# Kernel tuning notes

Hardware: AMD Instinct MI355X
Metric: run time of the kernel (lower is better)

Reference implementation:

```python
import jax, jax.numpy as jnp
import numpy as np

DK, DV, DMODEL, HEADNUM = 64, 64, 1024, 16
SEQ = 4096


def setup_inputs() -> dict:
    key = jax.random.key(0)
    ks = jax.random.split(key, 7)
    s = 0.02
    return {
        "q": jax.random.normal(ks[0], (SEQ, DMODEL), dtype=jnp.float32),
        "k": jax.random.normal(ks[1], (SEQ, DMODEL), dtype=jnp.float32),
        "v": jax.random.normal(ks[2], (SEQ, DMODEL), dtype=jnp.float32),
        # per-head projection weights, stored batched: [H, dmodel, dk]
        "Wq": jax.random.normal(ks[3], (HEADNUM, DMODEL, DK), dtype=jnp.float32) * s,
        "Wk": jax.random.normal(ks[4], (HEADNUM, DMODEL, DK), dtype=jnp.float32) * s,
        "Wv": jax.random.normal(ks[5], (HEADNUM, DMODEL, DV), dtype=jnp.float32) * s,
        # output linear (torch Linear weight [out, in]; y = x @ W.T)
        "Wo": jax.random.normal(ks[6], (DK * HEADNUM, DK * HEADNUM), dtype=jnp.float32) * s,
    }


def reference(q, k, v, Wq, Wk, Wv, Wo):
    # batched per-head projections: [H, S, dk/dv]
    qh = jnp.einsum("sd,hdk->hsk", q, Wq)
    kh = jnp.einsum("sd,hdk->hsk", k, Wk)
    vh = jnp.einsum("sd,hdv->hsv", v, Wv)
    scale = 1.0 / jnp.sqrt(jnp.asarray(DK, dtype=qh.dtype))
    scores = jnp.einsum("hqk,hsk->hqs", qh, kh) * scale  # [H, S, S]
    attn = jax.nn.softmax(scores, axis=-1)
    heads = jnp.einsum("hqs,hsv->hqv", attn, vh)  # [H, S, dv]
    # concat heads along feature dim: [S, H*dv]
    head_cat = jnp.transpose(heads, (1, 0, 2)).reshape(SEQ, HEADNUM * DV)
    return head_cat @ Wo.T
```

## Files before the change

### kernel.cpp

```cpp
#include <hip/hip_runtime.h>

#define SEQ 4096
#define DMODEL 1024
#define HEADNUM 16
#define DHEAD 64

typedef __attribute__((ext_vector_type(8))) short short8;
typedef __attribute__((ext_vector_type(4))) float f32x4;
typedef __attribute__((ext_vector_type(16))) float f32x16;
typedef __attribute__((ext_vector_type(4))) int i32x4;

__device__ __forceinline__ short f2bf(float f) {
    unsigned u = __float_as_uint(f);
    u = (u + 0x7fffu + ((u >> 16) & 1u)) >> 16;
    return (short)u;
}

__device__ __forceinline__ float bf2f(short s) {
    return __uint_as_float(((unsigned)(unsigned short)s) << 16);
}

__device__ __forceinline__ short8 cvt8(const float4 a, const float4 b) {
    short8 r;
    r[0] = f2bf(a.x); r[1] = f2bf(a.y); r[2] = f2bf(a.z); r[3] = f2bf(a.w);
    r[4] = f2bf(b.x); r[5] = f2bf(b.y); r[6] = f2bf(b.z); r[7] = f2bf(b.w);
    return r;
}

__device__ __forceinline__ int cvtpk_bf16(float lo, float hi) {
    int r;
    asm("v_cvt_pk_bf16_f32 %0, %1, %2" : "=v"(r) : "v"(lo), "v"(hi));
    return r;
}

__device__ __forceinline__ float fexp2(float x) {
    float r;
    asm("v_exp_f32 %0, %1" : "=v"(r) : "v"(x));
    return r;
}

__device__ __forceinline__ void perml32(int& a, int& b) {
    asm("v_permlane32_swap_b32 %0, %1" : "+v"(a), "+v"(b));
}

__device__ __forceinline__ void gld16(const void* g, void* l) {
    __builtin_amdgcn_global_load_lds(
        (const __attribute__((address_space(1))) void*)g,
        (__attribute__((address_space(3))) void*)l, 16, 0, 0);
}

__global__ __launch_bounds__(256) void prep_kernel(
    const float* __restrict__ q, const float* __restrict__ k,
    const float* __restrict__ v, const float* __restrict__ Wq,
    const float* __restrict__ Wk, const float* __restrict__ Wv,
    short* __restrict__ WT, short* __restrict__ qb,
    short* __restrict__ kb, short* __restrict__ vb) {
    int bid = blockIdx.x;
    int tid = threadIdx.x;
    __shared__ short tl[64][66];
    if (bid < 768) {
        int which = bid >> 8;
        int r = bid & 255;
        int h = r >> 4;
        int d0 = (r & 15) * 64;
        const float* W = which == 0 ? Wq : (which == 1 ? Wk : Wv);
        short* dst = WT + (size_t)which * (HEADNUM * DHEAD * DMODEL);
        int c = tid & 63, r4 = tid >> 6;
#pragma unroll
        for (int i = 0; i < 16; ++i) {
            int d = i * 4 + r4;
            tl[c][d] = f2bf(W[((size_t)h * DMODEL + d0 + d) * DHEAD + c]);
        }
        __syncthreads();
#pragma unroll
        for (int i = 0; i < 16; ++i) {
            int n = i * 4 + r4;
            dst[((size_t)h * DHEAD + n) * DMODEL + d0 + c] = tl[n][c];
        }
    } else {
        int i = (bid - 768) * 256 + tid;
        int seg = i >> 19;
        int off = i & ((1 << 19) - 1);
        const float* src = seg == 0 ? q : (seg == 1 ? k : v);
        short* dst = seg == 0 ? qb : (seg == 1 ? kb : vb);
        const float4* p = (const float4*)(src + (size_t)off * 8);
        *(short8*)(dst + (size_t)off * 8) = cvt8(p[0], p[1]);
    }
}

__device__ __forceinline__ void gemm_body(
    char* glds, const short* __restrict__ A, const short* __restrict__ Bw,
    short* __restrict__ outb, float* __restrict__ outf, int mode) {
    int b = blockIdx.x;
    int wgid = (b & 7) * 64 + (b >> 3);
    int bi = wgid >> 3;
    int ni = wgid & 7;
    int i0 = bi * 64, j0 = ni * 128;

    int tid = threadIdx.x;
    int lane = tid & 63;
    int wv = tid >> 6;
    int l15 = lane & 15;
    int g = lane >> 4;
    int wm = wv >> 1, wn = wv & 1;

    int ja0 = tid * 16, ja1 = ja0 + 4096;
    int sa0 = (ja0 >> 7) * 2048 + ((ja0 & 127) ^ (((ja0 >> 7) & 7) << 4));
    int sa1 = (ja1 >> 7) * 2048 + ((ja1 & 127) ^ (((ja1 >> 7) & 7) << 4));
    int jb0 = tid * 16, jb1 = jb0 + 4096, jb2 = jb0 + 8192, jb3 = jb0 + 12288;
    int sb0 = (jb0 >> 7) * 2048 + ((jb0 & 127) ^ (((jb0 >> 7) & 7) << 4));
    int sb1 = (jb1 >> 7) * 2048 + ((jb1 & 127) ^ (((jb1 >> 7) & 7) << 4));
    int sb2 = (jb2 >> 7) * 2048 + ((jb2 & 127) ^ (((jb2 >> 7) & 7) << 4));
    int sb3 = (jb3 >> 7) * 2048 + ((jb3 & 127) ^ (((jb3 >> 7) & 7) << 4));

    const char* Ab = (const char*)A + (size_t)i0 * 2048;
    const char* Bb = (const char*)Bw + (size_t)j0 * 2048;

#define GSTAGE(P, kt_)                          \
    {                                           \
        char* la_ = (P);                        \
        char* lb_ = (P) + 8192;                 \
        const char* As = Ab + (kt_) * 128;      \
        const char* Bs = Bb + (kt_) * 128;      \
        gld16(As + sa0, la_ + ja0);             \
        gld16(As + sa1, la_ + ja1);             \
        gld16(Bs + sb0, lb_ + jb0);             \
        gld16(Bs + sb1, lb_ + jb1);             \
        gld16(Bs + sb2, lb_ + jb2);             \
        gld16(Bs + sb3, lb_ + jb3);             \
    }

    f32x4 acc[2][4];
#pragma unroll
    for (int mm = 0; mm < 2; ++mm)
#pragma unroll
        for (int nn = 0; nn < 4; ++nn) acc[mm][nn] = (f32x4){0.f, 0.f, 0.f, 0.f};

#define GCOMPUTE(P)                                                                           \
    {                                                                                         \
        const char* la = (P);                                                                 \
        const char* lb = (P) + 8192;                                                          \
        _Pragma("unroll")                                                                     \
        for (int kc = 0; kc < 2; ++kc) {                                                      \
            short8 af[2], bf4[4];                                                             \
            _Pragma("unroll")                                                                 \
            for (int mm = 0; mm < 2; ++mm) {                                                  \
                int ra = wm * 32 + mm * 16 + l15;                                             \
                af[mm] = *(const short8*)(la + ra * 128 + ((kc * 64 + g * 16) ^ ((ra & 7) << 4))); \
            }                                                                                 \
            _Pragma("unroll")                                                                 \
            for (int nn = 0; nn < 4; ++nn) {                                                  \
                int rb = wn * 64 + nn * 16 + l15;                                             \
                bf4[nn] = *(const short8*)(lb + rb * 128 + ((kc * 64 + g * 16) ^ ((rb & 7) << 4))); \
            }                                                                                 \
            _Pragma("unroll")                                                                 \
            for (int mm = 0; mm < 2; ++mm)                                                    \
                _Pragma("unroll")                                                             \
                for (int nn = 0; nn < 4; ++nn)                                                \
                    acc[mm][nn] = __builtin_amdgcn_mfma_f32_16x16x32_bf16(af[mm], bf4[nn], acc[mm][nn], 0, 0, 0); \
        }                                                                                     \
    }

#define VMW(n) asm volatile("s_waitcnt vmcnt(" #n ")" ::: "memory")

    char* P0 = glds;
    char* P1 = glds + 24576;
    char* P2 = glds + 49152;
    GSTAGE(P0, 0);
    GSTAGE(P1, 1);
    for (int kt = 0; kt < 14; ++kt) {
        VMW(6);
        __builtin_amdgcn_s_barrier();
        GSTAGE(P2, kt + 2);
        GCOMPUTE(P0);
        char* tp = P0; P0 = P1; P1 = P2; P2 = tp;
    }
    VMW(6);
    __builtin_amdgcn_s_barrier();
    GCOMPUTE(P0);
    { char* tp = P0; P0 = P1; P1 = P2; P2 = tp; }
    VMW(0);
    __builtin_amdgcn_s_barrier();
    GCOMPUTE(P0);
#undef GSTAGE
#undef GCOMPUTE
#undef VMW

#pragma unroll
    for (int mm = 0; mm < 2; ++mm)
#pragma unroll
        for (int nn = 0; nn < 4; ++nn)
#pragma unroll
            for (int r = 0; r < 4; ++r) {
                int mg = i0 + wm * 32 + mm * 16 + 4 * g + r;
                int ng = j0 + wn * 64 + nn * 16 + l15;
                float val = acc[mm][nn][r];
                if (mode == 0)      outb[(size_t)mg * 1024 + ng] = f2bf(val);
                else if (mode == 1) outb[(size_t)ng * 4096 + mg] = f2bf(val);
                else                outf[(size_t)mg * 1024 + ng] = val;
            }
}

__global__ __launch_bounds__(256) void proj3_kernel(
    const short* __restrict__ qb, const short* __restrict__ kb,
    const short* __restrict__ vb, const short* __restrict__ WT,
    short* __restrict__ qh, short* __restrict__ kh, short* __restrict__ vt) {
    __shared__ __align__(16) char glds[3 * 24576];
    int which = blockIdx.y;
    const short* A = which == 0 ? qb : (which == 1 ? kb : vb);
    const short* B = WT + (size_t)which * (HEADNUM * DHEAD * DMODEL);
    short* outb = which == 0 ? qh : (which == 1 ? kh : vt);
    gemm_body(glds, A, B, outb, 0, which == 2 ? 1 : 0);
}

__global__ __launch_bounds__(256) void ogemm_kernel(
    const short* __restrict__ hc, const short* __restrict__ Wob,
    float* __restrict__ out) {
    __shared__ __align__(16) char glds[3 * 24576];
    gemm_body(glds, hc, Wob, 0, out, 2);
}

__global__ __launch_bounds__(256, 3) void attn_kernel(
    const short* __restrict__ qh, const short* __restrict__ kh,
    const short* __restrict__ vt, short* __restrict__ poA,
    short* __restrict__ poC, float* __restrict__ lbuf) {
    int b = blockIdx.x;
    int wg = (b & 7) * 96 + (b >> 3);
    int h = wg / 48;
    int rem = wg - h * 48;
    int split = rem >> 4;
    int qb = rem & 15;

    int tid = threadIdx.x;
    int lane = tid & 63;
    int wv = tid >> 6;
    int l31 = lane & 31;
    int hh = lane >> 5;
    int qbase = qb * 256 + wv * 64;
    int kv0 = split * 1376;
    int nt = (split < 2) ? 43 : 42;

    short* pob = (split < 2) ? poA + (size_t)split * SEQ * DMODEL : poC;

    __shared__ __align__(16) char lds_all[3 * 8192];

    const short* qpA = qh + (size_t)(qbase + l31) * 1024 + h * 64 + hh * 8;
    const short* qpB = qpA + 32 * 1024;
    short8 bqA0 = *(const short8*)(qpA);
    short8 bqA1 = *(const short8*)(qpA + 16);
    short8 bqA2 = *(const short8*)(qpA + 32);
    short8 bqA3 = *(const short8*)(qpA + 48);
    short8 bqB0 = *(const short8*)(qpB);
    short8 bqB1 = *(const short8*)(qpB + 16);
    short8 bqB2 = *(const short8*)(qpB + 32);
    short8 bqB3 = *(const short8*)(qpB + 48);

    const char* kbaseh = (const char*)kh + h * 128;
    const char* vbaseh = (const char*)vt + (size_t)h * 64 * 8192;

    int krow = tid >> 3;
    int kcol = (tid & 7) * 16;
    int ksrc = krow * 2048 + (kcol ^ ((krow & 7) << 4));
    int vrow = tid >> 2;
    int vswc = ((tid & 3) * 16) ^ (((vrow >> 1) & 3) << 4);
    size_t vsrcb = (size_t)vrow * 8192 + vswc;
    int ldst = tid * 16;

#define STAGE(P, kvg) {                                            \
    gld16(kbaseh + (size_t)(kvg) * 2048 + ksrc, (P) + ldst);       \
    gld16(vbaseh + (size_t)(kvg) * 2 + vsrcb, (P) + 4096 + ldst); }

    float lsumA = 0.f, lsumB = 0.f;
    f32x16 oaA0 = {}, oaA1 = {}, oaB0 = {}, oaB1 = {};

    int ksw = (l31 & 7) << 4;
    int hh16 = hh * 16;
    int vswz = (l31 >> 1) & 3;
    const float C1 = 0.18033688f;
    const float MB_ = 5.77078016f;

    char* p0 = lds_all;
    char* p1 = lds_all + 8192;
    char* p2 = lds_all + 16384;

    STAGE(p0, kv0);
    STAGE(p1, kv0 + 32);

#define VMW(n) asm volatile("s_waitcnt vmcnt(" #n ")" ::: "memory")

#define SOFTMAX(S, LSUM, PC0, PC1) {                                           \
    float e_[16];                                                              \
    _Pragma("unroll")                                                          \
    for (int i_ = 0; i_ < 16; ++i_) e_[i_] = fexp2(fmaf((S)[i_], C1, -MB_));   \
    LSUM += ((e_[0]+e_[1])+(e_[2]+e_[3])) + ((e_[4]+e_[5])+(e_[6]+e_[7]))      \
          + ((e_[8]+e_[9])+(e_[10]+e_[11])) + ((e_[12]+e_[13])+(e_[14]+e_[15])); \
    int pk0 = cvtpk_bf16(e_[0], e_[1]),   pk1 = cvtpk_bf16(e_[2], e_[3]);      \
    int pk2 = cvtpk_bf16(e_[4], e_[5]),   pk3 = cvtpk_bf16(e_[6], e_[7]);      \
    int pk4 = cvtpk_bf16(e_[8], e_[9]),   pk5 = cvtpk_bf16(e_[10], e_[11]);    \
    int pk6 = cvtpk_bf16(e_[12], e_[13]), pk7 = cvtpk_bf16(e_[14], e_[15]);    \
    perml32(pk0, pk2); perml32(pk1, pk3);                                      \
    perml32(pk4, pk6); perml32(pk5, pk7);                                      \
    i32x4 v0_; v0_[0] = pk0; v0_[1] = pk1; v0_[2] = pk2; v0_[3] = pk3;         \
    i32x4 v1_; v1_[0] = pk4; v1_[1] = pk5; v1_[2] = pk6; v1_[3] = pk7;         \
    PC0 = *(short8*)&v0_;                                                      \
    PC1 = *(short8*)&v1_; }

#define COMPUTE(KP) {                                                          \
    const char* kp_ = (KP);                                                    \
    const char* vp_ = (KP) + 4096;                                             \
    short8 ak0 = *(const short8*)(kp_ + l31 * 128 + ((0   + hh16) ^ ksw));     \
    short8 ak1 = *(const short8*)(kp_ + l31 * 128 + ((32  + hh16) ^ ksw));     \
    short8 ak2 = *(const short8*)(kp_ + l31 * 128 + ((64  + hh16) ^ ksw));     \
    short8 ak3 = *(const short8*)(kp_ + l31 * 128 + ((96  + hh16) ^ ksw));     \
    f32x16 sA = {}, sB = {};                                                   \
    __builtin_amdgcn_s_setprio(1);                                             \
    sA = __builtin_amdgcn_mfma_f32_32x32x16_bf16(ak0, bqA0, sA, 0, 0, 0);      \
    sA = __builtin_amdgcn_mfma_f32_32x32x16_bf16(ak1, bqA1, sA, 0, 0, 0);      \
    sA = __builtin_amdgcn_mfma_f32_32x32x16_bf16(ak2, bqA2, sA, 0, 0, 0);      \
    sA = __builtin_amdgcn_mfma_f32_32x32x16_bf16(ak3, bqA3, sA, 0, 0, 0);      \
    sB = __builtin_amdgcn_mfma_f32_32x32x16_bf16(ak0, bqB0, sB, 0, 0, 0);      \
    sB = __builtin_amdgcn_mfma_f32_32x32x16_bf16(ak1, bqB1, sB, 0, 0, 0);      \
    sB = __builtin_amdgcn_mfma_f32_32x32x16_bf16(ak2, bqB2, sB, 0, 0, 0);      \
    sB = __builtin_amdgcn_mfma_f32_32x32x16_bf16(ak3, bqB3, sB, 0, 0, 0);      \
    __builtin_amdgcn_s_setprio(0);                                             \
    short8 pcA0, pcA1, pcB0, pcB1;                                             \
    SOFTMAX(sA, lsumA, pcA0, pcA1);                                            \
    SOFTMAX(sB, lsumB, pcB0, pcB1);                                            \
    short8 av00 = *(const short8*)(vp_ + l31 * 64 + (((0 + hh) ^ vswz) << 4)); \
    short8 av01 = *(const short8*)(vp_ + l31 * 64 + (((2 + hh) ^ vswz) << 4)); \
    short8 av10 = *(const short8*)(vp_ + (32 + l31) * 64 + (((0 + hh) ^ vswz) << 4)); \
    short8 av11 = *(const short8*)(vp_ + (32 + l31) * 64 + (((2 + hh) ^ vswz) << 4)); \
    __builtin_amdgcn_s_setprio(1);                                             \
    oaA0 = __builtin_amdgcn_mfma_f32_32x32x16_bf16(av00, pcA0, oaA0, 0, 0, 0); \
    oaA0 = __builtin_amdgcn_mfma_f32_32x32x16_bf16(av01, pcA1, oaA0, 0, 0, 0); \
    oaA1 = __builtin_amdgcn_mfma_f32_32x32x16_bf16(av10, pcA0, oaA1, 0, 0, 0); \
    oaA1 = __builtin_amdgcn_mfma_f32_32x32x16_bf16(av11, pcA1, oaA1, 0, 0, 0); \
    oaB0 = __builtin_amdgcn_mfma_f32_32x32x16_bf16(av00, pcB0, oaB0, 0, 0, 0); \
    oaB0 = __builtin_amdgcn_mfma_f32_32x32x16_bf16(av01, pcB1, oaB0, 0, 0, 0); \
    oaB1 = __builtin_amdgcn_mfma_f32_32x32x16_bf16(av10, pcB0, oaB1, 0, 0, 0); \
    oaB1 = __builtin_amdgcn_mfma_f32_32x32x16_bf16(av11, pcB1, oaB1, 0, 0, 0); \
    __builtin_amdgcn_s_setprio(0); }

    for (int t = 0; t < nt - 2; ++t) {
        VMW(2);
        __builtin_amdgcn_s_barrier();
        STAGE(p2, kv0 + (t + 2) * 32);
        COMPUTE(p0);
        char* tp = p0; p0 = p1; p1 = p2; p2 = tp;
    }
    VMW(2);
    __builtin_amdgcn_s_barrier();
    COMPUTE(p0);
    { char* tp = p0; p0 = p1; p1 = p2; p2 = tp; }
    VMW(0);
    __builtin_amdgcn_s_barrier();
    COMPUTE(p0);
#undef COMPUTE
#undef SOFTMAX
#undef STAGE
#undef VMW

    {
        float ltA = lsumA + __shfl_xor(lsumA, 32);
        int qA = qbase + l31;
        if (hh == 0) lbuf[(size_t)(split * 16 + h) * 4096 + qA] = ltA;
        short* pr = pob + (size_t)qA * 1024 + h * 64 + hh * 4;
#pragma unroll
        for (int rp = 0; rp < 8; ++rp) {
            int dvb = ((2 * rp) & 3) + 8 * (rp >> 1);
            *(int*)(pr + dvb) = cvtpk_bf16(oaA0[2 * rp], oaA0[2 * rp + 1]);
            *(int*)(pr + 32 + dvb) = cvtpk_bf16(oaA1[2 * rp], oaA1[2 * rp + 1]);
        }
    }
    {
        float ltB = lsumB + __shfl_xor(lsumB, 32);
        int qB = qbase + 32 + l31;
        if (hh == 0) lbuf[(size_t)(split * 16 + h) * 4096 + qB] = ltB;
        short* pr = pob + (size_t)qB * 1024 + h * 64 + hh * 4;
#pragma unroll
        for (int rp = 0; rp < 8; ++rp) {
            int dvb = ((2 * rp) & 3) + 8 * (rp >> 1);
            *(int*)(pr + dvb) = cvtpk_bf16(oaB0[2 * rp], oaB0[2 * rp + 1]);
            *(int*)(pr + 32 + dvb) = cvtpk_bf16(oaB1[2 * rp], oaB1[2 * rp + 1]);
        }
    }
}

__global__ __launch_bounds__(256) void attn_reduce_kernel(
    const short* __restrict__ poA, const short* __restrict__ poC,
    const float* __restrict__ lbuf, short* __restrict__ hc,
    const float* __restrict__ Wo, short* __restrict__ Wob) {
    int bid = blockIdx.x;
    int tid = threadIdx.x;
    if (bid >= 2048) {
        int i = (bid - 2048) * 256 + tid;
        const float4* p = (const float4*)(Wo + (size_t)i * 8);
        *(short8*)(Wob + (size_t)i * 8) = cvt8(p[0], p[1]);
        return;
    }
    int idx = bid * 256 + tid;
    int q = idx >> 7;
    int cb = (idx & 127) * 8;
    int h = cb >> 6;
    float l = lbuf[(size_t)h * 4096 + q] + lbuf[(size_t)(16 + h) * 4096 + q] +
              lbuf[(size_t)(32 + h) * 4096 + q];
    float inv = 1.f / l;
    short8 a = *(const short8*)(poA + (size_t)q * 1024 + cb);
    short8 b2 = *(const short8*)(poA + (size_t)(4096 + q) * 1024 + cb);
    short8 c = *(const short8*)(poC + (size_t)q * 1024 + cb);
    short8 r;
#pragma unroll
    for (int j = 0; j < 8; ++j)
        r[j] = f2bf((bf2f(a[j]) + bf2f(b2[j]) + bf2f(c[j])) * inv);
    *(short8*)(hc + (size_t)q * 1024 + cb) = r;
}

extern "C" void kernel_launch(void* const* d_in, const int* in_sizes, int n_in,
                              void* d_out, int out_size, void* d_ws, size_t ws_size,
                              hipStream_t stream) {
    const float* q  = (const float*)d_in[0];
    const float* k  = (const float*)d_in[1];
    const float* v  = (const float*)d_in[2];
    const float* Wq = (const float*)d_in[3];
    const float* Wk = (const float*)d_in[4];
    const float* Wv = (const float*)d_in[5];
    const float* Wo = (const float*)d_in[6];
    float* out = (float*)d_out;

    char* ws = (char*)d_ws;
    const size_t MB = 1u << 20;
    short* WT   = (short*)(ws + 0 * MB);
    short* qh   = (short*)(ws + 6 * MB);
    short* kh   = (short*)(ws + 14 * MB);
    short* vt   = (short*)(ws + 22 * MB);
    short* qbws = (short*)(ws + 30 * MB);
    float* lbuf = (float*)(ws + 38 * MB);
    short* Wob  = WT;
    short* kb = (short*)d_out;
    short* vb = (short*)d_out + SEQ * DMODEL;
    short* poA = (short*)d_out;
    short* poC = qbws;
    short* hc = qh;

    prep_kernel<<<dim3(768 + 6144), 256, 0, stream>>>(
        q, k, v, Wq, Wk, Wv, WT, qbws, kb, vb);

    proj3_kernel<<<dim3(512, 3), 256, 0, stream>>>(qbws, kb, vb, WT, qh, kh, vt);

    attn_kernel<<<dim3(768), 256, 0, stream>>>(qh, kh, vt, poA, poC, lbuf);

    attn_reduce_kernel<<<dim3(2560), 256, 0, stream>>>(poA, poC, lbuf, hc, Wo, Wob);

    ogemm_kernel<<<dim3(512), 256, 0, stream>>>(hc, Wob, out);
}
```

Before: 168.2 us.

## Software-pipeline attention loop: overlap PV of previous tile with QK^T softmax

Splits the per-tile compute into a QK^T stage and a PV stage and skews them by one iteration. Each iteration's PV MFMAs for the previous tile can then interleave with the current tile's QK^T and softmax exp work. A fourth LDS buffer is added so the previous tile's V stays resident while new tiles stream in. This costs more LDS per block and live registers for the packed probabilities, which could lower occupancy.

```diff
diff --git a/kernel.cpp b/kernel.cpp
--- a/kernel.cpp
+++ b/kernel.cpp
@@ -242,7 +242,7 @@
 
     short* pob = (split < 2) ? poA + (size_t)split * SEQ * DMODEL : poC;
 
-    __shared__ __align__(16) char lds_all[3 * 8192];
+    __shared__ __align__(16) char lds_all[4 * 8192];
 
     const short* qpA = qh + (size_t)(qbase + l31) * 1024 + h * 64 + hh * 8;
     const short* qpB = qpA + 32 * 1024;
@@ -272,6 +272,7 @@
 
     float lsumA = 0.f, lsumB = 0.f;
     f32x16 oaA0 = {}, oaA1 = {}, oaB0 = {}, oaB1 = {};
+    short8 pcA0, pcA1, pcB0, pcB1;
 
     int ksw = (l31 & 7) << 4;
     int hh16 = hh * 16;
@@ -282,6 +283,7 @@
     char* p0 = lds_all;
     char* p1 = lds_all + 8192;
     char* p2 = lds_all + 16384;
+    char* p3 = lds_all + 24576;
 
     STAGE(p0, kv0);
     STAGE(p1, kv0 + 32);
@@ -305,27 +307,25 @@
     PC0 = *(short8*)&v0_;                                                      \
     PC1 = *(short8*)&v1_; }
 
-#define COMPUTE(KP) {                                                          \
+#define QKT(KP) {                                                              \
     const char* kp_ = (KP);                                                    \
-    const char* vp_ = (KP) + 4096;                                             \
     short8 ak0 = *(const short8*)(kp_ + l31 * 128 + ((0   + hh16) ^ ksw));     \
     short8 ak1 = *(const short8*)(kp_ + l31 * 128 + ((32  + hh16) ^ ksw));     \
     short8 ak2 = *(const short8*)(kp_ + l31 * 128 + ((64  + hh16) ^ ksw));     \
     short8 ak3 = *(const short8*)(kp_ + l31 * 128 + ((96  + hh16) ^ ksw));     \
-    f32x16 sA = {}, sB = {};                                                   \
     __builtin_amdgcn_s_setprio(1);                                             \
-    sA = __builtin_amdgcn_mfma_f32_32x32x16_bf16(ak0, bqA0, sA, 0, 0, 0);      \
-    sA = __builtin_amdgcn_mfma_f32_32x32x16_bf16(ak1, bqA1, sA, 0, 0, 0);      \
-    sA = __builtin_amdgcn_mfma_f32_32x32x16_bf16(ak2, bqA2, sA, 0, 0, 0);      \
-    sA = __builtin_amdgcn_mfma_f32_32x32x16_bf16(ak3, bqA3, sA, 0, 0, 0);      \
-    sB = __builtin_amdgcn_mfma_f32_32x32x16_bf16(ak0, bqB0, sB, 0, 0, 0);      \
-    sB = __builtin_amdgcn_mfma_f32_32x32x16_bf16(ak1, bqB1, sB, 0, 0, 0);      \
-    sB = __builtin_amdgcn_mfma_f32_32x32x16_bf16(ak2, bqB2, sB, 0, 0, 0);      \
-    sB = __builtin_amdgcn_mfma_f32_32x32x16_bf16(ak3, bqB3, sB, 0, 0, 0);      \
-    __builtin_amdgcn_s_setprio(0);                                             \
-    short8 pcA0, pcA1, pcB0, pcB1;                                             \
-    SOFTMAX(sA, lsumA, pcA0, pcA1);                                            \
-    SOFTMAX(sB, lsumB, pcB0, pcB1);                                            \
+    sA_ = __builtin_amdgcn_mfma_f32_32x32x16_bf16(ak0, bqA0, sA_, 0, 0, 0);    \
+    sA_ = __builtin_amdgcn_mfma_f32_32x32x16_bf16(ak1, bqA1, sA_, 0, 0, 0);    \
+    sA_ = __builtin_amdgcn_mfma_f32_32x32x16_bf16(ak2, bqA2, sA_, 0, 0, 0);    \
+    sA_ = __builtin_amdgcn_mfma_f32_32x32x16_bf16(ak3, bqA3, sA_, 0, 0, 0);    \
+    sB_ = __builtin_amdgcn_mfma_f32_32x32x16_bf16(ak0, bqB0, sB_, 0, 0, 0);    \
+    sB_ = __builtin_amdgcn_mfma_f32_32x32x16_bf16(ak1, bqB1, sB_, 0, 0, 0);    \
+    sB_ = __builtin_amdgcn_mfma_f32_32x32x16_bf16(ak2, bqB2, sB_, 0, 0, 0);    \
+    sB_ = __builtin_amdgcn_mfma_f32_32x32x16_bf16(ak3, bqB3, sB_, 0, 0, 0);    \
+    __builtin_amdgcn_s_setprio(0); }
+
+#define PVSTEP(VPB) {                                                          \
+    const char* vp_ = (VPB) + 4096;                                            \
     short8 av00 = *(const short8*)(vp_ + l31 * 64 + (((0 + hh) ^ vswz) << 4)); \
     short8 av01 = *(const short8*)(vp_ + l31 * 64 + (((2 + hh) ^ vswz) << 4)); \
     short8 av10 = *(const short8*)(vp_ + (32 + l31) * 64 + (((0 + hh) ^ vswz) << 4)); \
@@ -341,21 +341,53 @@
     oaB1 = __builtin_amdgcn_mfma_f32_32x32x16_bf16(av11, pcB1, oaB1, 0, 0, 0); \
     __builtin_amdgcn_s_setprio(0); }
 
-    for (int t = 0; t < nt - 2; ++t) {
+#define ROT4 { char* tp_ = p0; p0 = p1; p1 = p2; p2 = p3; p3 = tp_; }
+
+    {
+        VMW(2);
+        __builtin_amdgcn_s_barrier();
+        STAGE(p2, kv0 + 64);
+        f32x16 sA_ = {}, sB_ = {};
+        QKT(p0);
+        SOFTMAX(sA_, lsumA, pcA0, pcA1);
+        SOFTMAX(sB_, lsumB, pcB0, pcB1);
+        ROT4;
+    }
+    for (int t = 1; t <= nt - 3; ++t) {
         VMW(2);
         __builtin_amdgcn_s_barrier();
         STAGE(p2, kv0 + (t + 2) * 32);
-        COMPUTE(p0);
-        char* tp = p0; p0 = p1; p1 = p2; p2 = tp;
-    }
-    VMW(2);
-    __builtin_amdgcn_s_barrier();
-    COMPUTE(p0);
-    { char* tp = p0; p0 = p1; p1 = p2; p2 = tp; }
-    VMW(0);
-    __builtin_amdgcn_s_barrier();
-    COMPUTE(p0);
-#undef COMPUTE
+        f32x16 sA_ = {}, sB_ = {};
+        QKT(p0);
+        PVSTEP(p3);
+        SOFTMAX(sA_, lsumA, pcA0, pcA1);
+        SOFTMAX(sB_, lsumB, pcB0, pcB1);
+        ROT4;
+    }
+    {
+        VMW(2);
+        __builtin_amdgcn_s_barrier();
+        f32x16 sA_ = {}, sB_ = {};
+        QKT(p0);
+        PVSTEP(p3);
+        SOFTMAX(sA_, lsumA, pcA0, pcA1);
+        SOFTMAX(sB_, lsumB, pcB0, pcB1);
+        ROT4;
+    }
+    {
+        VMW(0);
+        __builtin_amdgcn_s_barrier();
+        f32x16 sA_ = {}, sB_ = {};
+        QKT(p0);
+        PVSTEP(p3);
+        SOFTMAX(sA_, lsumA, pcA0, pcA1);
+        SOFTMAX(sB_, lsumB, pcB0, pcB1);
+        ROT4;
+    }
+    PVSTEP(p3);
+#undef ROT4
+#undef PVSTEP
+#undef QKT
 #undef SOFTMAX
 #undef STAGE
 #undef VMW
```

Measured after the change: 181.0 us. +7.6%, slower.
